# Kernel tuning notes

Measured on AMD Instinct MI355X. Metric: run time of the kernel, lower is better.

## Reference

```python
import jax, jax.numpy as jnp
import numpy as np
import math

B, S, HID = 1, 2048, 2048
H, KVH, HD = 16, 4, 128
LEVEL = 256


def _rope_tables(seq_len, dim, dtype=jnp.float32):
    inv_freq = 1.0 / (10000.0 ** (np.arange(0, dim, 2, dtype=np.float32) / dim))
    ang = np.arange(seq_len, dtype=np.float32)[:, None] * inv_freq[None, :]  # [S, HD/2]
    emb = np.concatenate([ang, ang], axis=-1)  # [S, HD]
    return jnp.asarray(np.cos(emb), dtype)[None], jnp.asarray(np.sin(emb), dtype)[None]


def setup_inputs() -> dict:
    key = jax.random.key(0)
    ks = jax.random.split(key, 6)
    hidden_states = jax.random.normal(ks[0], (B, S, HID), jnp.float32)
    w_std = 1.0 / math.sqrt(HID)
    Wq = jax.random.normal(ks[1], (H * HD, HID), jnp.float32) * w_std
    Wk = jax.random.normal(ks[2], (KVH * HD, HID), jnp.float32) * w_std
    Wv = jax.random.normal(ks[3], (KVH * HD, HID), jnp.float32) * w_std
    Wo = jax.random.normal(ks[4], (HID, H * HD), jnp.float32) * w_std
    cos, sin = _rope_tables(S, HD)
    # additive causal mask [1,1,S,S]
    tri = jnp.tril(jnp.ones((S, S), jnp.bool_))
    attention_mask = jnp.where(tri, 0.0, -1e9).astype(jnp.float32)[None, None]
    return {
        "hidden_states": hidden_states,
        "Wq": Wq, "Wk": Wk, "Wv": Wv, "Wo": Wo,
        "s_q": jnp.full((1,), 0.05, jnp.float32),
        "s_k": jnp.full((1,), 0.05, jnp.float32),
        "s_v": jnp.full((1,), 0.05, jnp.float32),
        "s_attn": jnp.full((1,), 0.004, jnp.float32),
        "s_out": jnp.full((1,), 0.02, jnp.float32),
        "cos": cos, "sin": sin,
        "attention_mask": attention_mask,
    }


def _lsq(x, s, level, sym):
    # LSQ fake-quant: learned per-tensor step s, STE round, LSQ grad-scale on s.
    if sym:
        qn, qp = -level // 2, level // 2 - 1
    else:
        qn, qp = 0, level - 1
    g = 1.0 / math.sqrt(x.size * qp)          # LSQ gradient scale (static)
    s = jnp.abs(s)
    s_eff = s * g + jax.lax.stop_gradient(s - s * g)  # fwd = s, bwd grad *= g
    v = jnp.clip(x / s_eff, qn, qp)
    q = v + jax.lax.stop_gradient(jnp.round(v) - v)   # STE round
    return q * s_eff


def _rotate_half(x):
    x1, x2 = jnp.split(x, 2, axis=-1)
    return jnp.concatenate([-x2, x1], axis=-1)


def _attn_fwd(hidden_states, Wq, Wk, Wv, Wo, s_q, s_k, s_v, s_attn, s_out,
              cos, sin, attention_mask):
    b, s_len, _ = hidden_states.shape
    # projections -> [B, heads, S, HD]
    q = (hidden_states @ Wq.T).reshape(b, s_len, H, HD).transpose(0, 2, 1, 3)
    q = _lsq(q, s_q, LEVEL, sym=True)
    k = (hidden_states @ Wk.T).reshape(b, s_len, KVH, HD).transpose(0, 2, 1, 3)
    k = _lsq(k, s_k, LEVEL, sym=True)
    v = (hidden_states @ Wv.T).reshape(b, s_len, KVH, HD).transpose(0, 2, 1, 3)
    v = _lsq(v, s_v, LEVEL, sym=True)
    # RoPE (after quant, matching source order)
    c, si = cos[:, None], sin[:, None]  # [B,1,S,HD]
    q = q * c + _rotate_half(q) * si
    k = k * c + _rotate_half(k) * si
    # GQA repeat
    groups = H // KVH
    k = jnp.repeat(k, groups, axis=1)
    v = jnp.repeat(v, groups, axis=1)
    scores = jnp.einsum("bhqd,bhkd->bhqk", q, k) / math.sqrt(HD)
    scores = scores + attention_mask[:, :, :, :s_len]
    attn = jax.nn.softmax(scores.astype(jnp.float32), axis=-1).astype(q.dtype)
    attn = _lsq(attn, s_attn, LEVEL, sym=False)
    out = jnp.einsum("bhqk,bhkd->bhqd", attn, v)
    out = _lsq(out, s_out, LEVEL, sym=False)
    out = out.transpose(0, 2, 1, 3).reshape(b, s_len, H * HD)
    out = out @ Wo.T
    return out, attn


def reference(hidden_states, Wq, Wk, Wv, Wo, s_q, s_k, s_v, s_attn, s_out,
              cos, sin, attention_mask):
    return _attn_fwd(hidden_states, Wq, Wk, Wv, Wo, s_q, s_k, s_v, s_attn,
                     s_out, cos, sin, attention_mask)
```

## Files before the change

kernel.cpp:

```cpp
#include <hip/hip_runtime.h>
#include <math.h>

#define S_LEN 2048
#define HID_DIM 2048
#define NH 16
#define NKVH 4
#define HD 128
#define QD (NH*HD)
#define KD (NKVH*HD)
#define NQKV 3072

typedef _Float16 half8_t __attribute__((ext_vector_type(8)));
typedef _Float16 half4_t __attribute__((ext_vector_type(4)));
typedef float f32x4 __attribute__((ext_vector_type(4)));

#define BM 128
#define BN 128
#define BK 32

typedef const __attribute__((address_space(1))) char gas_char;
typedef __attribute__((address_space(3))) char las_char;
#define GL16(gp, lp) __builtin_amdgcn_global_load_lds((gas_char*)(gp), (las_char*)(lp), 16, 0, 0)

template<int LA, int LB, bool AF32>
__global__ __launch_bounds__(256)
void gemm_f16(const void* __restrict__ Ap, const _Float16* __restrict__ Alo,
              int lda, long long strA,
              const _Float16* __restrict__ Bhi, const _Float16* __restrict__ Blo,
              int ldb, long long strB, int divB,
              void* __restrict__ Cp, int ldc, long long strC,
              int K, float scale_c, const float* sc1, const float* sc2,
              const float* preAp,
              int qmode, const float* q1, const float* q2, const float* q3,
              int causal, int triK)
{
    int bz = blockIdx.z;
    int m0 = blockIdx.y * BM, n0 = blockIdx.x * BN;
    if (causal && n0 > m0 + (BM - 1)) return;
    int Keff = K;
    if (triK && (m0 + BM) < Keff) Keff = m0 + BM;

    const _Float16* Ahi = AF32 ? nullptr : (const _Float16*)Ap + bz * strA;
    const _Float16* AloP = (LA == 2) ? Alo + bz * strA : nullptr;
    const float* Af = AF32 ? (const float*)Ap + bz * strA : nullptr;
    const _Float16* BhiP = Bhi + (long long)(bz / divB) * strB;
    const _Float16* BloP = (LB == 2) ? Blo + (long long)(bz / divB) * strB : nullptr;
    float* Cf = (float*)Cp + bz * strC;
    _Float16* Ch = (_Float16*)Cp + bz * strC;

    float preA = 1.f;
    if (AF32) preA = 1.f / fabsf(preAp[0]);

    __shared__ _Float16 lds[(LA + LB) * 4096];
    _Float16* As0 = lds;
    _Float16* As1 = lds + 4096;
    _Float16* Bs0 = lds + LA * 4096;
    _Float16* Bs1 = lds + (LA + 1) * 4096;

    int t = threadIdx.x;
    int srow = t >> 2;
    int gsw = (srow >> 1) & 3;
    int gc = ((t & 3) ^ gsw) * 8;
    int w = t >> 6, lane = t & 63;
    int wm = (w >> 1) * 64, wn = (w & 1) * 64;
    int lr = lane & 15, lg = lane >> 4;
    int fco = ((lg ^ ((lr >> 1) & 3))) * 8;

    f32x4 acc[4][4];
    #pragma unroll
    for (int i = 0; i < 4; ++i)
        #pragma unroll
        for (int j = 0; j < 4; ++j)
            acc[i][j] = (f32x4){0.f, 0.f, 0.f, 0.f};

    for (int k0 = 0; k0 < Keff; k0 += BK) {
        f32x4 aF[2][2];
        if constexpr (AF32) {
            #pragma unroll
            for (int rep = 0; rep < 2; ++rep) {
                long long ai = (long long)(m0 + rep * 64 + srow) * lda + k0 + gc;
                aF[rep][0] = *(const f32x4*)&Af[ai];
                aF[rep][1] = *(const f32x4*)&Af[ai + 4];
            }
        }
        __syncthreads();
        #pragma unroll
        for (int rep = 0; rep < 2; ++rep) {
            int row = rep * 64 + srow;
            int lo = rep * 2048 + t * 8;
            if constexpr (!AF32) {
                long long ai = (long long)(m0 + row) * lda + k0 + gc;
                GL16(Ahi + ai, As0 + lo);
                if constexpr (LA == 2) GL16(AloP + ai, As1 + lo);
            }
            long long bi = (long long)(n0 + row) * ldb + k0 + gc;
            GL16(BhiP + bi, Bs0 + lo);
            if constexpr (LB == 2) GL16(BloP + bi, Bs1 + lo);
        }
        if constexpr (AF32) {
            #pragma unroll
            for (int rep = 0; rep < 2; ++rep) {
                half8_t h;
                #pragma unroll
                for (int e = 0; e < 4; ++e) {
                    h[e]     = (_Float16)(aF[rep][0][e] * preA);
                    h[e + 4] = (_Float16)(aF[rep][1][e] * preA);
                }
                *(half8_t*)&As0[rep * 2048 + t * 8] = h;
            }
        }
        __syncthreads();

        half8_t a0[4], b0[4];
        #pragma unroll
        for (int i = 0; i < 4; ++i) a0[i] = *(const half8_t*)&As0[(wm + i*16 + lr) * 32 + fco];
        #pragma unroll
        for (int j = 0; j < 4; ++j) b0[j] = *(const half8_t*)&Bs0[(wn + j*16 + lr) * 32 + fco];
        #pragma unroll
        for (int i = 0; i < 4; ++i)
            #pragma unroll
            for (int j = 0; j < 4; ++j)
                acc[i][j] = __builtin_amdgcn_mfma_f32_16x16x32_f16(a0[i], b0[j], acc[i][j], 0, 0, 0);
        if constexpr (LB == 2) {
            half8_t b1[4];
            #pragma unroll
            for (int j = 0; j < 4; ++j) b1[j] = *(const half8_t*)&Bs1[(wn + j*16 + lr) * 32 + fco];
            #pragma unroll
            for (int i = 0; i < 4; ++i)
                #pragma unroll
                for (int j = 0; j < 4; ++j)
                    acc[i][j] = __builtin_amdgcn_mfma_f32_16x16x32_f16(a0[i], b1[j], acc[i][j], 0, 0, 0);
        }
        if constexpr (LA == 2) {
            half8_t a1[4];
            #pragma unroll
            for (int i = 0; i < 4; ++i) a1[i] = *(const half8_t*)&As1[(wm + i*16 + lr) * 32 + fco];
            #pragma unroll
            for (int i = 0; i < 4; ++i)
                #pragma unroll
                for (int j = 0; j < 4; ++j)
                    acc[i][j] = __builtin_amdgcn_mfma_f32_16x16x32_f16(a1[i], b0[j], acc[i][j], 0, 0, 0);
        }
    }

    float se = scale_c;
    if (sc1) se *= fabsf(sc1[0]);
    if (sc2) se *= fabsf(sc2[0]);
    float sv = 1.f;
    if (qmode == 3) {
        const float* sp = (n0 < 2048) ? q1 : ((n0 < 2560) ? q2 : q3);
        sv = fabsf(sp[0]);
        qmode = 1;
    } else if (qmode) {
        sv = fabsf(q1[0]);
    }

    #pragma unroll
    for (int i = 0; i < 4; ++i)
        #pragma unroll
        for (int j = 0; j < 4; ++j)
            #pragma unroll
            for (int r = 0; r < 4; ++r) {
                long long row = m0 + wm + i * 16 + lg * 4 + r;
                long long col = n0 + wn + j * 16 + lr;
                float v = acc[i][j][r] * se;
                if (qmode == 0) {
                    Cf[row * (long long)ldc + col] = v;
                } else if (qmode == 1) {
                    float u = rintf(fminf(fmaxf(v / sv, -128.f), 127.f));
                    Ch[row * (long long)ldc + col] = (_Float16)u;
                } else {
                    float u = rintf(fminf(fmaxf(v / sv, 0.f), 255.f));
                    Ch[row * (long long)ldc + col] = (_Float16)u;
                }
            }
}

__global__ __launch_bounds__(256)
void scores_gemm(const _Float16* __restrict__ qhi, const _Float16* __restrict__ qlo,
                 const _Float16* __restrict__ khi, const _Float16* __restrict__ klo,
                 float* __restrict__ attn, float* __restrict__ pml,
                 const float* sq_p, const float* sk_p)
{
    int m0 = blockIdx.y * BM, n0 = blockIdx.x * BN;
    if (n0 > m0 + (BM - 1)) return;
    int h = blockIdx.z;

    const _Float16* Ahi = qhi + (long long)h * S_LEN * HD;
    const _Float16* Alo = qlo + (long long)h * S_LEN * HD;
    const _Float16* Bhi = khi + (long long)(h >> 2) * S_LEN * HD;
    const _Float16* Blo = klo + (long long)(h >> 2) * S_LEN * HD;
    float* S = attn + (long long)h * S_LEN * S_LEN;

    float se = fabsf(sq_p[0]) * fabsf(sk_p[0]) * 0.08838834764831845f;

    __shared__ float lds_f[8448];
    _Float16* As0 = (_Float16*)lds_f;
    _Float16* As1 = As0 + 4096;
    _Float16* Bs0 = As0 + 8192;
    _Float16* Bs1 = As0 + 12288;

    int t = threadIdx.x;
    int srow = t >> 2;
    int gsw = (srow >> 1) & 3;
    int gc = ((t & 3) ^ gsw) * 8;
    int w = t >> 6, lane = t & 63;
    int wm = (w >> 1) * 64, wn = (w & 1) * 64;
    int lr = lane & 15, lg = lane >> 4;
    int fco = ((lg ^ ((lr >> 1) & 3))) * 8;

    f32x4 acc[4][4];
    #pragma unroll
    for (int i = 0; i < 4; ++i)
        #pragma unroll
        for (int j = 0; j < 4; ++j)
            acc[i][j] = (f32x4){0.f, 0.f, 0.f, 0.f};

    for (int k0 = 0; k0 < HD; k0 += BK) {
        __syncthreads();
        #pragma unroll
        for (int rep = 0; rep < 2; ++rep) {
            int row = rep * 64 + srow;
            int lo = rep * 2048 + t * 8;
            long long ai = (long long)(m0 + row) * HD + k0 + gc;
            long long bi = (long long)(n0 + row) * HD + k0 + gc;
            GL16(Ahi + ai, As0 + lo);
            GL16(Alo + ai, As1 + lo);
            GL16(Bhi + bi, Bs0 + lo);
            GL16(Blo + bi, Bs1 + lo);
        }
        __syncthreads();

        half8_t a0[4], b0[4], a1[4], b1[4];
        #pragma unroll
        for (int i = 0; i < 4; ++i) {
            a0[i] = *(const half8_t*)&As0[(wm + i*16 + lr) * 32 + fco];
            a1[i] = *(const half8_t*)&As1[(wm + i*16 + lr) * 32 + fco];
        }
        #pragma unroll
        for (int j = 0; j < 4; ++j) {
            b0[j] = *(const half8_t*)&Bs0[(wn + j*16 + lr) * 32 + fco];
            b1[j] = *(const half8_t*)&Bs1[(wn + j*16 + lr) * 32 + fco];
        }
        #pragma unroll
        for (int i = 0; i < 4; ++i)
            #pragma unroll
            for (int j = 0; j < 4; ++j)
                acc[i][j] = __builtin_amdgcn_mfma_f32_16x16x32_f16(a0[i], b0[j], acc[i][j], 0, 0, 0);
        #pragma unroll
        for (int i = 0; i < 4; ++i)
            #pragma unroll
            for (int j = 0; j < 4; ++j)
                acc[i][j] = __builtin_amdgcn_mfma_f32_16x16x32_f16(a0[i], b1[j], acc[i][j], 0, 0, 0);
        #pragma unroll
        for (int i = 0; i < 4; ++i)
            #pragma unroll
            for (int j = 0; j < 4; ++j)
                acc[i][j] = __builtin_amdgcn_mfma_f32_16x16x32_f16(a1[i], b0[j], acc[i][j], 0, 0, 0);
    }

    int cb64 = (n0 + wn) >> 6;
    #pragma unroll
    for (int i = 0; i < 4; ++i)
        #pragma unroll
        for (int r = 0; r < 4; ++r) {
            int row = m0 + wm + i * 16 + lg * 4 + r;
            float vv[4];
            float mloc = -INFINITY;
            #pragma unroll
            for (int j = 0; j < 4; ++j) {
                int col = n0 + wn + j * 16 + lr;
                float v = acc[i][j][r] * se;
                vv[j] = (col <= row) ? v : -INFINITY;
                mloc = fmaxf(mloc, vv[j]);
            }
            #pragma unroll
            for (int o = 1; o < 16; o <<= 1) mloc = fmaxf(mloc, __shfl_xor(mloc, o));
            float sloc = 0.f;
            #pragma unroll
            for (int j = 0; j < 4; ++j) sloc += __expf(vv[j] - mloc);
            #pragma unroll
            for (int o = 1; o < 16; o <<= 1) sloc += __shfl_xor(sloc, o);
            if (lr == 0) {
                long long idx = (((long long)h * S_LEN + row) * 32 + cb64) * 2;
                pml[idx] = mloc;
                pml[idx + 1] = sloc;
            }
        }

    int r_own = wm >> 6;
    int lrow = t >> 5;
    int lcol = (t & 31) * 4;
    #pragma unroll
    for (int half = 0; half < 2; ++half) {
        __syncthreads();
        if (r_own == half) {
            #pragma unroll
            for (int i = 0; i < 4; ++i)
                #pragma unroll
                for (int j = 0; j < 4; ++j)
                    #pragma unroll
                    for (int r = 0; r < 4; ++r)
                        lds_f[(i * 16 + lg * 4 + r) * 132 + wn + j * 16 + lr] = acc[i][j][r] * se;
        }
        __syncthreads();
        #pragma unroll
        for (int it = 0; it < 8; ++it) {
            int row = it * 8 + lrow;
            f32x4 v = *(const f32x4*)&lds_f[row * 132 + lcol];
            *(f32x4*)&S[(long long)(m0 + half * 64 + row) * S_LEN + n0 + lcol] = v;
        }
    }
}

__global__ __launch_bounds__(256)
void reduce_ml(const float* __restrict__ pml, float* __restrict__ fml)
{
    int id = blockIdx.x * 256 + threadIdx.x;
    int r = id & (S_LEN - 1);
    int nb = (r >> 6) + 1;
    float m = -INFINITY, l = 0.f;
    const float* p = pml + (long long)id * 64;
    for (int cb = 0; cb < nb; ++cb) {
        float mp = p[cb * 2], lp = p[cb * 2 + 1];
        float mn = fmaxf(m, mp);
        l = l * __expf(m - mn) + lp * __expf(mp - mn);
        m = mn;
    }
    fml[id * 2] = m;
    fml[id * 2 + 1] = l;
}

__global__ __launch_bounds__(256)
void finalize_quant(float* __restrict__ attn, const float* __restrict__ fml,
                    const float* __restrict__ s_at_p)
{
    int row = blockIdx.x;
    int q = row & (S_LEN - 1);
    float* p = attn + (long long)row * S_LEN;
    float m = fml[row * 2];
    float l = fml[row * 2 + 1];
    float sa = fabsf(s_at_p[0]);
    int t = threadIdx.x;
    int n4 = (q + 4) & ~3;
    for (int c = t * 4; c < n4; c += 1024) {
        f32x4 v = *(const f32x4*)&p[c];
        f32x4 o;
        #pragma unroll
        for (int e = 0; e < 4; ++e) {
            float u = 0.f;
            if (c + e <= q) {
                float pr = __expf(v[e] - m) / l;
                u = rintf(fminf(fmaxf(pr / sa, 0.f), 255.f));
            }
            o[e] = u * sa;
        }
        *(f32x4*)&p[c] = o;
    }
    f32x4 z = (f32x4){0.f, 0.f, 0.f, 0.f};
    for (int c = n4 + t * 4; c < S_LEN; c += 1024)
        *(f32x4*)&p[c] = z;
}

__global__ void split_f16(const float* __restrict__ in, _Float16* __restrict__ hi,
                          _Float16* __restrict__ lo, int n4)
{
    int i = blockIdx.x * 256 + threadIdx.x;
    if (i >= n4) return;
    f32x4 v = ((const f32x4*)in)[i];
    half4_t h, l;
    #pragma unroll
    for (int e = 0; e < 4; ++e) {
        h[e] = (_Float16)v[e];
        l[e] = (_Float16)(v[e] - (float)h[e]);
    }
    ((half4_t*)hi)[i] = h;
    ((half4_t*)lo)[i] = l;
}

__global__ void rope_f16(const _Float16* __restrict__ codes, int ldc_, int colOff,
                         const float* __restrict__ cosT,
                         const float* __restrict__ sinT,
                         _Float16* __restrict__ ohi, _Float16* __restrict__ olo, int nh)
{
    long long idx = (long long)blockIdx.x * 256 + threadIdx.x;
    int d = idx & (HD - 1);
    long long tt = idx >> 7;
    int h = (int)(tt % nh);
    int s = (int)(tt / nh);
    long long base = (long long)s * ldc_ + colOff + h * HD;
    float x = (float)codes[base + d];
    float other = (d < 64) ? -(float)codes[base + d + 64] : (float)codes[base + d - 64];
    float o = x * cosT[s * HD + d] + other * sinT[s * HD + d];
    _Float16 hf = (_Float16)o;
    long long oi = ((long long)h * S_LEN + s) * HD + d;
    ohi[oi] = hf;
    olo[oi] = (_Float16)(o - (float)hf);
}

__global__ __launch_bounds__(256)
void transpose_vf16(const _Float16* __restrict__ in, _Float16* __restrict__ outp)
{
    __shared__ _Float16 tile[64][72];
    int s0 = blockIdx.x * 64, d0 = blockIdx.y * 64, h = blockIdx.z;
    int t = threadIdx.x;
    int rr = t >> 4, cc = (t & 15) * 4;
    #pragma unroll
    for (int r = 0; r < 4; ++r) {
        half4_t v = *(const half4_t*)&in[(long long)(s0 + rr + 16*r) * NQKV + 2560 + h * HD + d0 + cc];
        *(half4_t*)&tile[rr + 16*r][cc] = v;
    }
    __syncthreads();
    #pragma unroll
    for (int r = 0; r < 4; ++r) {
        int dr = rr + 16 * r;
        half4_t o = { tile[cc+0][dr], tile[cc+1][dr], tile[cc+2][dr], tile[cc+3][dr] };
        *(half4_t*)&outp[((long long)h * HD + d0 + dr) * S_LEN + s0 + cc] = o;
    }
}

extern "C" void kernel_launch(void* const* d_in, const int* in_sizes, int n_in,
                              void* d_out, int out_size, void* d_ws, size_t ws_size,
                              hipStream_t stream)
{
    const float* hs    = (const float*)d_in[0];
    const float* Wq    = (const float*)d_in[1];
    const float* Wk    = (const float*)d_in[2];
    const float* Wv    = (const float*)d_in[3];
    const float* Wo    = (const float*)d_in[4];
    const float* s_q   = (const float*)d_in[5];
    const float* s_k   = (const float*)d_in[6];
    const float* s_v   = (const float*)d_in[7];
    const float* s_at  = (const float*)d_in[8];
    const float* s_out = (const float*)d_in[9];
    const float* cosT  = (const float*)d_in[10];
    const float* sinT  = (const float*)d_in[11];

    float* out  = (float*)d_out;
    float* attn = out + (long long)S_LEN * HID_DIM;

    const long long M1 = 1LL * 1024 * 1024;
    const long long M4 = 4LL * M1;
    const long long M6 = 6LL * M1;

    _Float16* wsh   = (_Float16*)d_ws;
    _Float16* qr_hi = wsh;
    _Float16* qr_lo = qr_hi + M4;
    _Float16* kr_hi = qr_lo + M4;
    _Float16* kr_lo = kr_hi + M1;
    _Float16* vT    = kr_lo + M1;
    _Float16* ao    = vT + M1;
    _Float16* Wo_hi = ao + M4;
    _Float16* Wo_lo = Wo_hi + M4;

    _Float16* sc      = (_Float16*)attn;
    _Float16* hs_hi   = sc;
    _Float16* hs_lo   = hs_hi + M4;
    _Float16* Whi     = hs_lo + M4;
    _Float16* Wlo     = Whi + M6;
    _Float16* qkvcode = Wlo + M6;

    float* pml = out;
    float* fml = out + 2LL * 1024 * 1024;

    dim3 blk(256);

    split_f16<<<4096, blk, 0, stream>>>(hs, hs_hi, hs_lo, 1024*1024);
    split_f16<<<4096, blk, 0, stream>>>(Wq, Whi, Wlo, 1024*1024);
    split_f16<<<1024, blk, 0, stream>>>(Wk, Whi + 2048LL*2048, Wlo + 2048LL*2048, 256*1024);
    split_f16<<<1024, blk, 0, stream>>>(Wv, Whi + 2560LL*2048, Wlo + 2560LL*2048, 256*1024);
    split_f16<<<4096, blk, 0, stream>>>(Wo, Wo_hi, Wo_lo, 1024*1024);

    gemm_f16<2,2,false><<<dim3(NQKV/BN, S_LEN/BM, 1), blk, 0, stream>>>(
        hs_hi, hs_lo, HID_DIM, 0, Whi, Wlo, HID_DIM, 0, 1,
        qkvcode, NQKV, 0, HID_DIM, 1.f, nullptr, nullptr, nullptr,
        3, s_q, s_k, s_v, 0, 0);

    rope_f16<<<(NH*S_LEN*HD)/256, blk, 0, stream>>>(qkvcode, NQKV, 0, cosT, sinT, qr_hi, qr_lo, NH);
    rope_f16<<<(NKVH*S_LEN*HD)/256, blk, 0, stream>>>(qkvcode, NQKV, 2048, cosT, sinT, kr_hi, kr_lo, NKVH);
    transpose_vf16<<<dim3(S_LEN/64, HD/64, NKVH), blk, 0, stream>>>(qkvcode, vT);

    scores_gemm<<<dim3(S_LEN/BN, S_LEN/BM, NH), blk, 0, stream>>>(
        qr_hi, qr_lo, kr_hi, kr_lo, attn, pml, s_q, s_k);

    reduce_ml<<<(NH*S_LEN)/256, blk, 0, stream>>>(pml, fml);

    finalize_quant<<<NH*S_LEN, blk, 0, stream>>>(attn, fml, s_at);

    gemm_f16<1,1,true><<<dim3(1, S_LEN/BM, NH), blk, 0, stream>>>(
        attn, nullptr, S_LEN, (long long)S_LEN*S_LEN,
        vT, nullptr, S_LEN, (long long)HD*S_LEN, NH/NKVH,
        ao, QD, HD,
        S_LEN, 1.f, s_at, s_v, s_at, 2, s_out, nullptr, nullptr, 0, 1);

    gemm_f16<1,2,false><<<dim3(HID_DIM/BN, S_LEN/BM, 1), blk, 0, stream>>>(
        ao, nullptr, QD, 0, Wo_hi, Wo_lo, QD, 0, 1,
        out, HID_DIM, 0, QD, 1.f, s_out, nullptr, nullptr,
        0, nullptr, nullptr, nullptr, 0, 0);
}
```

Before: 504.1 us.

## Fuse softmax finalize and quantization into the PV GEMM kernel

Removes the separate finalize_quant pass over the full attention matrix. The new pv_fused kernel reads raw scores, applies the exp/normalize/quantize step while staging the A tile into LDS, writes the dequantized attention back, and runs the MFMA PV product in the same pass, limited to the causal K range. Upper-triangle zeroing moves into scores_gemm's early-exit blocks. The fused kernel has a single LDS buffer with no double buffering and only NH*16 blocks, so latency hiding and occupancy may be weak.

```diff
diff --git a/kernel.cpp b/kernel.cpp
--- a/kernel.cpp
+++ b/kernel.cpp
@@ -183,14 +183,23 @@
                  const float* sq_p, const float* sk_p)
 {
     int m0 = blockIdx.y * BM, n0 = blockIdx.x * BN;
-    if (n0 > m0 + (BM - 1)) return;
     int h = blockIdx.z;
+    float* S = attn + (long long)h * S_LEN * S_LEN;
+    int t = threadIdx.x;
+
+    if (n0 > m0 + (BM - 1)) {
+        int zrow = t >> 5, zcol = (t & 31) * 4;
+        f32x4 z = (f32x4){0.f, 0.f, 0.f, 0.f};
+        #pragma unroll
+        for (int it = 0; it < 16; ++it)
+            *(f32x4*)&S[(long long)(m0 + it * 8 + zrow) * S_LEN + n0 + zcol] = z;
+        return;
+    }
 
     const _Float16* Ahi = qhi + (long long)h * S_LEN * HD;
     const _Float16* Alo = qlo + (long long)h * S_LEN * HD;
     const _Float16* Bhi = khi + (long long)(h >> 2) * S_LEN * HD;
     const _Float16* Blo = klo + (long long)(h >> 2) * S_LEN * HD;
-    float* S = attn + (long long)h * S_LEN * S_LEN;
 
     float se = fabsf(sq_p[0]) * fabsf(sk_p[0]) * 0.08838834764831845f;
 
@@ -200,7 +209,6 @@
     _Float16* Bs0 = As0 + 8192;
     _Float16* Bs1 = As0 + 12288;
 
-    int t = threadIdx.x;
     int srow = t >> 2;
     int gsw = (srow >> 1) & 3;
     int gc = ((t & 3) ^ gsw) * 8;
@@ -332,34 +340,110 @@
 }
 
 __global__ __launch_bounds__(256)
-void finalize_quant(float* __restrict__ attn, const float* __restrict__ fml,
-                    const float* __restrict__ s_at_p)
-{
-    int row = blockIdx.x;
-    int q = row & (S_LEN - 1);
-    float* p = attn + (long long)row * S_LEN;
-    float m = fml[row * 2];
-    float l = fml[row * 2 + 1];
-    float sa = fabsf(s_at_p[0]);
+void pv_fused(float* __restrict__ attn, const _Float16* __restrict__ vT,
+              const float* __restrict__ fml, _Float16* __restrict__ ao,
+              const float* sa_p, const float* sv_p, const float* so_p)
+{
+    int h = blockIdx.z;
+    int m0 = blockIdx.y * BM;
+    int Keff = m0 + BM;
+    float* S = attn + (long long)h * S_LEN * S_LEN;
+    const _Float16* B = vT + (long long)(h >> 2) * HD * S_LEN;
+
+    float sa = fabsf(sa_p[0]);
+    float se = sa * fabsf(sv_p[0]);
+    float so = fabsf(so_p[0]);
+
+    __shared__ _Float16 lds[8192];
+    _Float16* As0 = lds;
+    _Float16* Bs0 = lds + 4096;
+
     int t = threadIdx.x;
-    int n4 = (q + 4) & ~3;
-    for (int c = t * 4; c < n4; c += 1024) {
-        f32x4 v = *(const f32x4*)&p[c];
-        f32x4 o;
-        #pragma unroll
-        for (int e = 0; e < 4; ++e) {
-            float u = 0.f;
-            if (c + e <= q) {
-                float pr = __expf(v[e] - m) / l;
-                u = rintf(fminf(fmaxf(pr / sa, 0.f), 255.f));
-            }
-            o[e] = u * sa;
-        }
-        *(f32x4*)&p[c] = o;
-    }
-    f32x4 z = (f32x4){0.f, 0.f, 0.f, 0.f};
-    for (int c = n4 + t * 4; c < S_LEN; c += 1024)
-        *(f32x4*)&p[c] = z;
+    int srow = t >> 2;
+    int gsw = (srow >> 1) & 3;
+    int gc = ((t & 3) ^ gsw) * 8;
+    int w = t >> 6, lane = t & 63;
+    int wm = (w >> 1) * 64, wn = (w & 1) * 64;
+    int lr = lane & 15, lg = lane >> 4;
+    int fco = ((lg ^ ((lr >> 1) & 3))) * 8;
+
+    float mrow[2], lrow[2];
+    #pragma unroll
+    for (int rep = 0; rep < 2; ++rep) {
+        long long id = (long long)h * S_LEN + m0 + rep * 64 + srow;
+        mrow[rep] = fml[id * 2];
+        lrow[rep] = fml[id * 2 + 1];
+    }
+
+    f32x4 acc[4][4];
+    #pragma unroll
+    for (int i = 0; i < 4; ++i)
+        #pragma unroll
+        for (int j = 0; j < 4; ++j)
+            acc[i][j] = (f32x4){0.f, 0.f, 0.f, 0.f};
+
+    for (int k0 = 0; k0 < Keff; k0 += BK) {
+        f32x4 aF[2][2];
+        #pragma unroll
+        for (int rep = 0; rep < 2; ++rep) {
+            long long ai = (long long)(m0 + rep * 64 + srow) * S_LEN + k0 + gc;
+            aF[rep][0] = *(const f32x4*)&S[ai];
+            aF[rep][1] = *(const f32x4*)&S[ai + 4];
+        }
+        __syncthreads();
+        #pragma unroll
+        for (int rep = 0; rep < 2; ++rep) {
+            long long bi = (long long)(rep * 64 + srow) * S_LEN + k0 + gc;
+            GL16(B + bi, Bs0 + rep * 2048 + t * 8);
+        }
+        #pragma unroll
+        for (int rep = 0; rep < 2; ++rep) {
+            int row = m0 + rep * 64 + srow;
+            half8_t hc;
+            f32x4 o0, o1;
+            #pragma unroll
+            for (int e = 0; e < 8; ++e) {
+                int col = k0 + gc + e;
+                float v = (e < 4) ? aF[rep][0][e] : aF[rep][1][e - 4];
+                float u = 0.f;
+                if (col <= row) {
+                    float pr = __expf(v - mrow[rep]) / lrow[rep];
+                    u = rintf(fminf(fmaxf(pr / sa, 0.f), 255.f));
+                }
+                hc[e] = (_Float16)u;
+                if (e < 4) o0[e] = u * sa; else o1[e - 4] = u * sa;
+            }
+            *(half8_t*)&As0[rep * 2048 + t * 8] = hc;
+            long long ai = (long long)row * S_LEN + k0 + gc;
+            *(f32x4*)&S[ai] = o0;
+            *(f32x4*)&S[ai + 4] = o1;
+        }
+        __syncthreads();
+
+        half8_t a0[4], b0[4];
+        #pragma unroll
+        for (int i = 0; i < 4; ++i) a0[i] = *(const half8_t*)&As0[(wm + i*16 + lr) * 32 + fco];
+        #pragma unroll
+        for (int j = 0; j < 4; ++j) b0[j] = *(const half8_t*)&Bs0[(wn + j*16 + lr) * 32 + fco];
+        #pragma unroll
+        for (int i = 0; i < 4; ++i)
+            #pragma unroll
+            for (int j = 0; j < 4; ++j)
+                acc[i][j] = __builtin_amdgcn_mfma_f32_16x16x32_f16(a0[i], b0[j], acc[i][j], 0, 0, 0);
+    }
+
+    #pragma unroll
+    for (int i = 0; i < 4; ++i)
+        #pragma unroll
+        for (int j = 0; j < 4; ++j)
+            #pragma unroll
+            for (int r = 0; r < 4; ++r) {
+                long long row = m0 + wm + i * 16 + lg * 4 + r;
+                int d = wn + j * 16 + lr;
+                float v = acc[i][j][r] * se;
+                float u = rintf(fminf(fmaxf(v / so, 0.f), 255.f));
+                ao[row * (long long)QD + h * HD + d] = (_Float16)u;
+            }
 }
 
 __global__ void split_f16(const float* __restrict__ in, _Float16* __restrict__ hi,
@@ -485,13 +569,8 @@
 
     reduce_ml<<<(NH*S_LEN)/256, blk, 0, stream>>>(pml, fml);
 
-    finalize_quant<<<NH*S_LEN, blk, 0, stream>>>(attn, fml, s_at);
-
-    gemm_f16<1,1,true><<<dim3(1, S_LEN/BM, NH), blk, 0, stream>>>(
-        attn, nullptr, S_LEN, (long long)S_LEN*S_LEN,
-        vT, nullptr, S_LEN, (long long)HD*S_LEN, NH/NKVH,
-        ao, QD, HD,
-        S_LEN, 1.f, s_at, s_v, s_at, 2, s_out, nullptr, nullptr, 0, 1);
+    pv_fused<<<dim3(1, S_LEN/BM, NH), blk, 0, stream>>>(
+        attn, vT, fml, ao, s_at, s_v, s_out);
 
     gemm_f16<1,2,false><<<dim3(HID_DIM/BN, S_LEN/BM, 1), blk, 0, stream>>>(
         ao, nullptr, QD, 0, Wo_hi, Wo_lo, QD, 0, 1,
```

Measured after the change: 511.5 us. About the same (+1.5%).
